# Kernel optimization log

Hardware: AMD Instinct MI355X
Metric: run time of the kernel (lower is better)

## Reference

```python
import jax, jax.numpy as jnp
import numpy as np

N_NODES = 50000
N_EDGES = 800000
IN_C = 128
OUT_C = 128


def setup_inputs() -> dict:
    key = jax.random.key(0)
    k1, k2, k3 = jax.random.split(key, 3)
    x = jax.random.normal(k1, (N_NODES, IN_C), dtype=jnp.float32)
    edge_index = jax.random.randint(k2, (2, N_EDGES), 0, N_NODES, dtype=jnp.int64)
    weight = jax.random.normal(k3, (IN_C, OUT_C), dtype=jnp.float32) * 0.01
    bias = jnp.zeros((OUT_C,), dtype=jnp.float32)
    return {"x": x, "edge_index": edge_index, "weight": weight, "bias": bias}


def reference(x, edge_index, weight, bias):
    num_nodes = x.shape[0]
    # add self-loops
    loop = jnp.arange(num_nodes, dtype=edge_index.dtype)
    src = jnp.concatenate([edge_index[0], loop])  # [E + N]
    dst = jnp.concatenate([edge_index[1], loop])  # [E + N]
    # in-degree (incl. self-loops) via scatter-add
    deg = jax.ops.segment_sum(jnp.ones_like(dst, dtype=x.dtype), dst,
                              num_segments=num_nodes)
    # deg >= 1 due to self-loops, but guard inf like the original
    deg_inv_sqrt = jnp.where(deg > 0, jax.lax.rsqrt(deg), 0.0)
    norm = deg_inv_sqrt[src] * deg_inv_sqrt[dst]  # [E + N]
    x_transformed = x @ weight  # [N, out_c]
    messages = x_transformed[src] * norm[:, None]  # [E + N, out_c]
    out = jax.ops.segment_sum(messages, dst, num_segments=num_nodes)
    return out + bias
```

## Files before the change

kernel.cpp:

```cpp
#include <hip/hip_runtime.h>

#define C 128
#define CHUNK 3200
#define K4CAP 5120

typedef short bf16x8 __attribute__((ext_vector_type(8)));
typedef float f32x4 __attribute__((ext_vector_type(4)));

__device__ inline unsigned short f2bf(float f) {
    unsigned u = __float_as_uint(f);
    u += 0x7fffu + ((u >> 16) & 1u);
    return (unsigned short)(u >> 16);
}

__device__ inline unsigned pk2bf(float lo, float hi) {
    return (unsigned)f2bf(lo) | ((unsigned)f2bf(hi) << 16);
}

__global__ __launch_bounds__(256) void kfused(
        const int* __restrict__ ei, int e,
        int* __restrict__ cur, unsigned* __restrict__ staging,
        int nblocks, int nbuck,
        const float* __restrict__ W, unsigned short* __restrict__ Wt) {
    int b = blockIdx.x;
    int t = threadIdx.x;
    if (b >= nblocks) {
        int i = (b - nblocks) * 256 + t;
        int nn = i >> 7, k = i & 127;
        Wt[nn * 128 + k] = f2bf(W[k * 128 + nn]);
        return;
    }
    __shared__ int sdst[CHUNK];
    __shared__ int ssrc[CHUNK];
    __shared__ int h[256];
    __shared__ int c[256];
    h[t] = 0;
    __syncthreads();
    int base = b * CHUNK;
    int lim = min(CHUNK, e - base);
    for (int i = t; i < lim; i += 256) {
        int s = ei[base + i];
        int d = ei[e + base + i];
        ssrc[i] = s;
        sdst[i] = d;
        atomicAdd(&h[d >> 8], 1);
    }
    __syncthreads();
    if (t < nbuck) {
        int cnt = h[t];
        c[t] = cnt ? atomicAdd(&cur[t], cnt) : 0;
    }
    __syncthreads();
    for (int i = t; i < lim; i += 256) {
        int s = ssrc[i];
        int d = sdst[i];
        int g = d >> 8;
        int pos = atomicAdd(&c[g], 1);
        if (pos < K4CAP)
            staging[(size_t)g * K4CAP + pos] = (unsigned)s | ((unsigned)(d & 255) << 16);
    }
}

__global__ __launch_bounds__(256) void k4_finalize(
        const unsigned* __restrict__ staging, const int* __restrict__ cur,
        int2* __restrict__ row_se, float* __restrict__ dis,
        unsigned short* __restrict__ srcs, int n) {
    __shared__ unsigned rec[K4CAP];
    __shared__ int sc[256];
    __shared__ int cu[256];
    int g = blockIdx.x, t = threadIdx.x;
    int cnt = min(cur[g], K4CAP);
    int s0 = g * K4CAP;
    sc[t] = 0;
    __syncthreads();
    for (int li = t; li < cnt; li += 256) {
        unsigned r = staging[s0 + li];
        rec[li] = r;
        atomicAdd(&sc[r >> 16], 1);
    }
    __syncthreads();
    int v = sc[t];
    __syncthreads();
    for (int off = 1; off < 256; off <<= 1) {
        int u = (t >= off) ? sc[t - off] : 0;
        __syncthreads();
        sc[t] += u;
        __syncthreads();
    }
    int excl = sc[t] - v;
    int idx = g * 256 + t;
    if (idx < n) {
        row_se[idx] = make_int2(s0 + excl, s0 + excl + v);
        dis[idx] = rsqrtf((float)(v + 1));
    }
    cu[t] = s0 + excl;
    __syncthreads();
    for (int li = t; li < cnt; li += 256) {
        unsigned r = rec[li];
        int pos = atomicAdd(&cu[r >> 16], 1);
        srcs[pos] = (unsigned short)(r & 0xffffu);
    }
}

__global__ __launch_bounds__(256) void gemm_mfma(
        const float* __restrict__ x, const unsigned short* __restrict__ Wt,
        const float* __restrict__ dis, unsigned short* __restrict__ xts, int n) {
    const int lane = threadIdx.x & 63;
    const int wave = threadIdx.x >> 6;
    const int m = lane & 15;
    const int q = lane >> 4;
    const int r0 = blockIdx.x * 64 + wave * 16;
    const int row = r0 + m;
    const int rowc = (row < n) ? row : (n - 1);

    f32x4 acc[8];
#pragma unroll
    for (int nt = 0; nt < 8; ++nt) acc[nt] = (f32x4){0.f, 0.f, 0.f, 0.f};

#pragma unroll
    for (int kb = 0; kb < 4; ++kb) {
        const int k0 = kb * 32 + q * 8;
        const float4* xp = (const float4*)(x + (size_t)rowc * 128 + k0);
        float4 xa = xp[0];
        float4 xb = xp[1];
        union { unsigned u[4]; bf16x8 v; } af;
        af.u[0] = pk2bf(xa.x, xa.y);
        af.u[1] = pk2bf(xa.z, xa.w);
        af.u[2] = pk2bf(xb.x, xb.y);
        af.u[3] = pk2bf(xb.z, xb.w);
#pragma unroll
        for (int nt = 0; nt < 8; ++nt) {
            bf16x8 bf = *(const bf16x8*)(Wt + (size_t)(nt * 16 + m) * 128 + k0);
            acc[nt] = __builtin_amdgcn_mfma_f32_16x16x32_bf16(af.v, bf, acc[nt], 0, 0, 0);
        }
    }

    float dv[4];
    int gr[4];
#pragma unroll
    for (int r = 0; r < 4; ++r) {
        gr[r] = r0 + q * 4 + r;
        dv[r] = dis[(gr[r] < n) ? gr[r] : (n - 1)];
    }
#pragma unroll
    for (int nt = 0; nt < 8; ++nt) {
        int col = nt * 16 + m;
#pragma unroll
        for (int r = 0; r < 4; ++r) {
            if (gr[r] < n)
                xts[(size_t)gr[r] * 128 + col] = f2bf(acc[nt][r] * dv[r]);
        }
    }
}

__device__ inline void acc8(float* a, uint4 w) {
    a[0] += __uint_as_float(w.x << 16);
    a[1] += __uint_as_float(w.x & 0xffff0000u);
    a[2] += __uint_as_float(w.y << 16);
    a[3] += __uint_as_float(w.y & 0xffff0000u);
    a[4] += __uint_as_float(w.z << 16);
    a[5] += __uint_as_float(w.z & 0xffff0000u);
    a[6] += __uint_as_float(w.w << 16);
    a[7] += __uint_as_float(w.w & 0xffff0000u);
}

__global__ void gather3(const int2* __restrict__ row_se,
                        const unsigned short* __restrict__ srcs,
                        const unsigned short* __restrict__ xts,
                        const float* __restrict__ dis,
                        const float* __restrict__ bias, float* __restrict__ out, int n) {
    int node = blockIdx.x * 16 + (threadIdx.x >> 4);
    int q = threadIdx.x & 15;
    if (node >= n) return;
    const uint4* x4 = (const uint4*)xts;
    int2 se = row_se[node];
    int start = se.x;
    int end = se.y;
    float a0[8] = {0, 0, 0, 0, 0, 0, 0, 0};
    float a1[8] = {0, 0, 0, 0, 0, 0, 0, 0};
    acc8(a0, x4[node * 16 + q]);
    int j = start;
    for (; j + 4 <= end; j += 4) {
        int s0 = srcs[j], s1 = srcs[j + 1], s2 = srcs[j + 2], s3 = srcs[j + 3];
        uint4 m0 = x4[s0 * 16 + q];
        uint4 m1 = x4[s1 * 16 + q];
        uint4 m2 = x4[s2 * 16 + q];
        uint4 m3 = x4[s3 * 16 + q];
        acc8(a0, m0);
        acc8(a1, m1);
        acc8(a0, m2);
        acc8(a1, m3);
    }
    for (; j < end; ++j) acc8(a0, x4[(int)srcs[j] * 16 + q]);
    float d = dis[node];
    const float4 b0 = ((const float4*)bias)[q * 2];
    const float4 b1 = ((const float4*)bias)[q * 2 + 1];
    float4 o0, o1;
    o0.x = (a0[0] + a1[0]) * d + b0.x;
    o0.y = (a0[1] + a1[1]) * d + b0.y;
    o0.z = (a0[2] + a1[2]) * d + b0.z;
    o0.w = (a0[3] + a1[3]) * d + b0.w;
    o1.x = (a0[4] + a1[4]) * d + b1.x;
    o1.y = (a0[5] + a1[5]) * d + b1.y;
    o1.z = (a0[6] + a1[6]) * d + b1.z;
    o1.w = (a0[7] + a1[7]) * d + b1.w;
    float4* op = (float4*)(out + node * 128 + q * 8);
    op[0] = o0;
    op[1] = o1;
}

extern "C" void kernel_launch(void* const* d_in, const int* in_sizes, int n_in,
                              void* d_out, int out_size, void* d_ws, size_t ws_size,
                              hipStream_t stream) {
    const float* x    = (const float*)d_in[0];
    const int*   ei   = (const int*)d_in[1];
    const float* W    = (const float*)d_in[2];
    const float* bias = (const float*)d_in[3];
    float* out = (float*)d_out;

    const int n = in_sizes[0] / C;
    const int e = in_sizes[1] / 2;
    const int nblocks = (e + CHUNK - 1) / CHUNK;
    const int nbuck = (n + 255) >> 8;
    const int G = (n + 63) / 64;

    char* p = (char*)d_ws;
    auto alloc = [&](size_t bytes) {
        char* r = p;
        p += (bytes + 15) & ~(size_t)15;
        return (void*)r;
    };
    int*      cur     = (int*)alloc(nbuck * 4);
    unsigned* staging = (unsigned*)alloc((size_t)nbuck * K4CAP * 4);
    int2*     row_se  = (int2*)alloc((size_t)n * 8);
    float*    dis     = (float*)alloc(n * 4);
    unsigned short* srcs = (unsigned short*)alloc((size_t)nbuck * K4CAP * 2);
    unsigned short* xts  = (unsigned short*)alloc((size_t)n * C * 2);
    unsigned short* Wt   = (unsigned short*)alloc(128 * 128 * 2);

    hipMemsetAsync(cur, 0, nbuck * 4, stream);
    kfused<<<nblocks + 64, 256, 0, stream>>>(ei, e, cur, staging, nblocks,
                                             nbuck, W, Wt);
    k4_finalize<<<nbuck, 256, 0, stream>>>(staging, cur, row_se, dis, srcs, n);
    gemm_mfma<<<G, 256, 0, stream>>>(x, Wt, dis, xts, n);
    gather3<<<(n + 15) / 16, 256, 0, stream>>>(row_se, srcs, xts, dis, bias, out, n);
}
```

Before: 162.3 us.

## Gather each node with a full wave, splitting edges across four lane groups

The gather kernel now assigns one 64-lane wave per node instead of 16 lanes per node. The four 16-lane groups take interleaved edges (stride 4, two in flight each) and combine partial sums with cross-lane shuffles. Two groups then write the output halves. This cuts the serial edge loop per lane and aims to raise memory-level parallelism across nodes with uneven degree, at the cost of shuffle reductions, idle lanes on low-degree nodes, and four times as many blocks.

```diff
diff --git a/kernel.cpp b/kernel.cpp
--- a/kernel.cpp
+++ b/kernel.cpp
@@ -164,49 +164,55 @@
     a[7] += __uint_as_float(w.w & 0xffff0000u);
 }
 
-__global__ void gather3(const int2* __restrict__ row_se,
+__global__ void gather4(const int2* __restrict__ row_se,
                         const unsigned short* __restrict__ srcs,
                         const unsigned short* __restrict__ xts,
                         const float* __restrict__ dis,
                         const float* __restrict__ bias, float* __restrict__ out, int n) {
-    int node = blockIdx.x * 16 + (threadIdx.x >> 4);
-    int q = threadIdx.x & 15;
+    int node = blockIdx.x * 4 + (threadIdx.x >> 6);
     if (node >= n) return;
+    int lane = threadIdx.x & 63;
+    int e = lane >> 4, q = lane & 15;
     const uint4* x4 = (const uint4*)xts;
     int2 se = row_se[node];
-    int start = se.x;
     int end = se.y;
     float a0[8] = {0, 0, 0, 0, 0, 0, 0, 0};
     float a1[8] = {0, 0, 0, 0, 0, 0, 0, 0};
-    acc8(a0, x4[node * 16 + q]);
-    int j = start;
-    for (; j + 4 <= end; j += 4) {
-        int s0 = srcs[j], s1 = srcs[j + 1], s2 = srcs[j + 2], s3 = srcs[j + 3];
+    if (e == 0) acc8(a0, x4[node * 16 + q]);
+    int j = se.x + e;
+    for (; j + 4 < end; j += 8) {
+        int s0 = srcs[j], s1 = srcs[j + 4];
         uint4 m0 = x4[s0 * 16 + q];
         uint4 m1 = x4[s1 * 16 + q];
-        uint4 m2 = x4[s2 * 16 + q];
-        uint4 m3 = x4[s3 * 16 + q];
         acc8(a0, m0);
         acc8(a1, m1);
-        acc8(a0, m2);
-        acc8(a1, m3);
-    }
-    for (; j < end; ++j) acc8(a0, x4[(int)srcs[j] * 16 + q]);
+    }
+    if (j < end) acc8(a0, x4[(int)srcs[j] * 16 + q]);
+#pragma unroll
+    for (int i = 0; i < 8; ++i) a0[i] += a1[i];
+#pragma unroll
+    for (int i = 0; i < 8; ++i) {
+        a0[i] += __shfl_xor(a0[i], 16, 64);
+        a0[i] += __shfl_xor(a0[i], 32, 64);
+    }
     float d = dis[node];
-    const float4 b0 = ((const float4*)bias)[q * 2];
-    const float4 b1 = ((const float4*)bias)[q * 2 + 1];
-    float4 o0, o1;
-    o0.x = (a0[0] + a1[0]) * d + b0.x;
-    o0.y = (a0[1] + a1[1]) * d + b0.y;
-    o0.z = (a0[2] + a1[2]) * d + b0.z;
-    o0.w = (a0[3] + a1[3]) * d + b0.w;
-    o1.x = (a0[4] + a1[4]) * d + b1.x;
-    o1.y = (a0[5] + a1[5]) * d + b1.y;
-    o1.z = (a0[6] + a1[6]) * d + b1.z;
-    o1.w = (a0[7] + a1[7]) * d + b1.w;
-    float4* op = (float4*)(out + node * 128 + q * 8);
-    op[0] = o0;
-    op[1] = o1;
+    if (e == 0) {
+        const float4 b = ((const float4*)bias)[q * 2];
+        float4 o;
+        o.x = a0[0] * d + b.x;
+        o.y = a0[1] * d + b.y;
+        o.z = a0[2] * d + b.z;
+        o.w = a0[3] * d + b.w;
+        ((float4*)(out + (size_t)node * 128))[q * 2] = o;
+    } else if (e == 1) {
+        const float4 b = ((const float4*)bias)[q * 2 + 1];
+        float4 o;
+        o.x = a0[4] * d + b.x;
+        o.y = a0[5] * d + b.y;
+        o.z = a0[6] * d + b.z;
+        o.w = a0[7] * d + b.w;
+        ((float4*)(out + (size_t)node * 128))[q * 2 + 1] = o;
+    }
 }
 
 extern "C" void kernel_launch(void* const* d_in, const int* in_sizes, int n_in,
@@ -243,5 +249,5 @@
                                              nbuck, W, Wt);
     k4_finalize<<<nbuck, 256, 0, stream>>>(staging, cur, row_se, dis, srcs, n);
     gemm_mfma<<<G, 256, 0, stream>>>(x, Wt, dis, xts, n);
-    gather3<<<(n + 15) / 16, 256, 0, stream>>>(row_se, srcs, xts, dis, bias, out, n);
-}
+    gather4<<<(n + 3) / 4, 256, 0, stream>>>(row_se, srcs, xts, dis, bias, out, n);
+}
```

Result: no change. 161.8 us (-0.3%).
